# Performance work log

Hardware: AMD Instinct MI355X
Metric: run time of the kernel (lower is better)

The kernel has to match this reference:

```python
import jax, jax.numpy as jnp
import numpy as np

N_NODES = 100000
N_EDGES = 1600000
IN_DIM = 33
HID = 128
N_CLASSES = 10
N_GRAPHS = 128


def _glorot(key, shape):
    fan_in, fan_out = shape[0], shape[1]
    lim = (6.0 / (fan_in + fan_out)) ** 0.5
    return jax.random.uniform(key, shape, jnp.float32, -lim, lim)


def setup_inputs() -> dict:
    key = jax.random.key(0)
    ks = jax.random.split(key, 20)
    x = jax.random.normal(ks[0], (N_NODES, IN_DIM), jnp.float32)
    edge_index = jax.random.randint(ks[1], (2, N_EDGES), 0, N_NODES, jnp.int64)
    edge_w = jax.random.uniform(ks[2], (N_EDGES,), jnp.float32)
    batch = jnp.sort(jax.random.randint(ks[3], (N_NODES,), 0, N_GRAPHS, jnp.int64))
    p = {
        "We": _glorot(ks[4], (IN_DIM, HID)), "be": jnp.zeros((HID,), jnp.float32),
        "W1": _glorot(ks[5], (HID, HID)), "b1": jnp.zeros((HID,), jnp.float32),
        "W2": _glorot(ks[6], (HID, HID)), "b2": jnp.zeros((HID,), jnp.float32),
        "W3": _glorot(ks[7], (HID, HID)), "b3": jnp.zeros((HID,), jnp.float32),
        "W4": _glorot(ks[8], (HID, HID)), "b4": jnp.zeros((HID,), jnp.float32),
        "Wr1": _glorot(ks[9], (HID, HID // 2)), "br1": jnp.zeros((HID // 2,), jnp.float32),
        "Wr2": _glorot(ks[10], (HID // 2, HID // 4)), "br2": jnp.zeros((HID // 4,), jnp.float32),
        "Wr3": _glorot(ks[11], (HID // 4, N_CLASSES)),
    }
    return dict(x=x, edge_index=edge_index, edge_w=edge_w, batch=batch, **p)


def reference(x, edge_index, edge_w, batch,
              We, be, W1, b1, W2, b2, W3, b3, W4, b4,
              Wr1, br1, Wr2, br2, Wr3):
    N = x.shape[0]
    row, col = edge_index[0], edge_index[1]
    # PyG gcn_norm with add_self_loops=True: append (i,i) edges with weight 1
    loop = jnp.arange(N)
    row2 = jnp.concatenate([row, loop])
    col2 = jnp.concatenate([col, loop])
    w2 = jnp.concatenate([edge_w, jnp.ones((N,), edge_w.dtype)])
    deg = jax.ops.segment_sum(w2, col2, num_segments=N)  # in-degree incl. self-loop
    dinv = jnp.where(deg > 0, deg ** -0.5, 0.0)
    norm = dinv[row2] * w2 * dinv[col2]  # [E+N] symmetric normalization

    def conv(h, W, b):
        h = h @ W  # linear transform first (PyG GCNConv)
        msg = norm[:, None] * h[row2]  # gather + scale
        return jax.ops.segment_sum(msg, col2, num_segments=N) + b  # scatter-add to targets

    h = x @ We + be
    h = jax.nn.relu(conv(h, W1, b1))
    h = jax.nn.relu(conv(h, W2, b2))
    h = jax.nn.relu(conv(h, W3, b3))
    h = jax.nn.relu(conv(h, W4, b4))

    # global mean pool over graphs
    sums = jax.ops.segment_sum(h, batch, num_segments=N_GRAPHS)
    cnt = jax.ops.segment_sum(jnp.ones((N,), h.dtype), batch, num_segments=N_GRAPHS)
    pooled = sums / jnp.maximum(cnt, 1.0)[:, None]  # [G, HID]

    r = jax.nn.relu(pooled @ Wr1 + br1)
    r = jax.nn.relu(r @ Wr2 + br2)
    return r @ Wr3  # [G, n_classes]
```

## Files before the change

kernel.cpp:

```cpp
#include <hip/hip_runtime.h>
#include <hip/hip_bf16.h>

#define NN 100000
#define NE 1600000
#define IN_DIM 33
#define HID 128
#define NG 128
#define NCLS 10

using short8 = __attribute__((ext_vector_type(8))) short;
using floatx4 = __attribute__((ext_vector_type(4))) float;

static __device__ __forceinline__ size_t szmul(int a, int b) {
    return (size_t)a * (size_t)b;
}

static __device__ __forceinline__ unsigned short f2bf(float f) {
    unsigned u = __float_as_uint(f);
    u += 0x7fffu + ((u >> 16) & 1u);
    return (unsigned short)(u >> 16);
}
static __device__ __forceinline__ float bf_lo(unsigned u) { return __uint_as_float(u << 16); }
static __device__ __forceinline__ float bf_hi(unsigned u) { return __uint_as_float(u & 0xffff0000u); }

__global__ void k_init(int* bucket_cnt, int* bucket_fill, float* gsum) {
    int i = blockIdx.x * blockDim.x + threadIdx.x;
    if (i < 513) { bucket_cnt[i] = 0; bucket_fill[i] = 0; }
    if (i < NG * HID) gsum[i] = 0.0f;
}


__global__ __launch_bounds__(256) void k_bhist(const int* __restrict__ col,
                                               int* __restrict__ bucket_cnt, int e, int nbk) {
    __shared__ int hist[512];
    int tid = threadIdx.x;
    for (int i = tid; i < nbk; i += 256) hist[i] = 0;
    __syncthreads();
    for (int i = blockIdx.x * 256 + tid; i < e; i += 256 * 256)
        atomicAdd(&hist[col[i] >> 8], 1);
    __syncthreads();
    for (int i = tid; i < nbk; i += 256)
        if (hist[i]) atomicAdd(&bucket_cnt[i], hist[i]);
}

__global__ void k_scan_small(int* data, int nb) {
    __shared__ int s[512];
    int t = threadIdx.x;
    int v = (t < nb) ? data[t] : 0;
    s[t] = v;
    __syncthreads();
    for (int o = 1; o < 512; o <<= 1) {
        int a = (t >= o) ? s[t - o] : 0;
        __syncthreads();
        s[t] += a;
        __syncthreads();
    }
    if (t < nb) data[t] = s[t] - v;
    if (t == nb - 1) data[nb] = s[t];
}

__global__ __launch_bounds__(256) void k_bin_scatter(const int* __restrict__ row,
                                                     const int* __restrict__ col,
                                                     const float* __restrict__ w,
                                                     const int* __restrict__ bucket_base,
                                                     int* __restrict__ bucket_fill,
                                                     uint2* __restrict__ binned, int e, int nbk) {
    __shared__ int hist[512], rnk[512], basub[512];
    int tid = threadIdx.x;
    int c0 = blockIdx.x * 4096;
    for (int i = tid; i < nbk; i += 256) { hist[i] = 0; rnk[i] = 0; }
    __syncthreads();
    int myb[16]; unsigned myp[16]; unsigned myw[16];
#pragma unroll
    for (int u = 0; u < 16; ++u) {
        int idx = c0 + u * 256 + tid;
        int b = -1;
        if (idx < e) {
            int c = col[idx];
            int r = row[idx];
            myw[u] = __float_as_uint(w[idx]);
            b = c >> 8;
            myp[u] = ((unsigned)(c & 255) << 17) | (unsigned)r;
            atomicAdd(&hist[b], 1);
        }
        myb[u] = b;
    }
    __syncthreads();
    for (int i = tid; i < nbk; i += 256) {
        int c = hist[i];
        basub[i] = (c > 0) ? (bucket_base[i] + atomicAdd(&bucket_fill[i], c)) : 0;
    }
    __syncthreads();
#pragma unroll
    for (int u = 0; u < 16; ++u) {
        int b = myb[u];
        if (b >= 0) {
            int rk = atomicAdd(&rnk[b], 1);
            binned[basub[b] + rk] = make_uint2(myp[u], myw[u]);
        }
    }
}

__global__ __launch_bounds__(256) void k_bucket_cnt(const uint2* __restrict__ binned,
                                                    const int* __restrict__ bucket_base,
                                                    int* __restrict__ cnt, int n) {
    __shared__ int c256[256];
    int b = blockIdx.x, tid = threadIdx.x;
    c256[tid] = 0;
    __syncthreads();
    int beg = bucket_base[b], end = bucket_base[b + 1];
    for (int e2 = beg + tid; e2 < end; e2 += 256)
        atomicAdd(&c256[(binned[e2].x >> 17) & 255], 1);
    __syncthreads();
    int node = b * 256 + tid;
    if (node < n) cnt[node] = c256[tid];
}

#define SCAN_B 1024
__global__ void k_scan1(const int* __restrict__ cnt, int* __restrict__ rowptr,
                        int* __restrict__ bsums, int n) {
    __shared__ int s[SCAN_B];
    int t = threadIdx.x;
    int i = blockIdx.x * SCAN_B + t;
    int v = (i < n) ? cnt[i] : 0;
    s[t] = v;
    __syncthreads();
    for (int o = 1; o < SCAN_B; o <<= 1) {
        int a = (t >= o) ? s[t - o] : 0;
        __syncthreads();
        s[t] += a;
        __syncthreads();
    }
    if (i < n) rowptr[i] = s[t] - v;
    if (t == SCAN_B - 1) bsums[blockIdx.x] = s[t];
}

__global__ void k_scan3(int* rowptr, const int* __restrict__ bsums, int n, int etot) {
    int i = blockIdx.x * blockDim.x + threadIdx.x;
    if (i < n) rowptr[i] += bsums[i >> 10];
    else if (i == n) rowptr[n] = etot;
}

__global__ __launch_bounds__(256) void k_bucket_scatter(const uint2* __restrict__ binned,
                                                        const int* __restrict__ bucket_base,
                                                        const int* __restrict__ rowptr,
                                                        int2* __restrict__ csr, int n) {
    __shared__ int f256[256];
    int b = blockIdx.x, tid = threadIdx.x;
    f256[tid] = 0;
    __syncthreads();
    int beg = bucket_base[b], end = bucket_base[b + 1];
    for (int e2 = beg + tid; e2 < end; e2 += 256) {
        uint2 rec = binned[e2];
        int lo = (rec.x >> 17) & 255;
        int node = (b << 8) | lo;
        int src = rec.x & 0x1FFFF;
        int pos = rowptr[node] + atomicAdd(&f256[lo], 1);
        csr[pos] = make_int2(src, (int)rec.y);
    }
    (void)n;
}

__global__ void k_deg(const int* __restrict__ rowptr, const int2* __restrict__ csr,
                      float* __restrict__ dinv, float* __restrict__ selfn, int n) {
    int i = blockIdx.x * blockDim.x + threadIdx.x;
    if (i >= n) return;
    int beg = rowptr[i], end = rowptr[i + 1];
    float d = 1.0f;
    for (int e = beg; e < end; ++e) d += __int_as_float(csr[e].y);
    float di = (d > 0.0f) ? (1.0f / sqrtf(d)) : 0.0f;
    dinv[i] = di;
    selfn[i] = di * di;
}

__global__ void k_norm(const int* __restrict__ rowptr, int2* __restrict__ csr,
                       const float* __restrict__ dinv, int n) {
    int i = blockIdx.x * blockDim.x + threadIdx.x;
    if (i >= n) return;
    float dc = dinv[i];
    int beg = rowptr[i], end = rowptr[i + 1];
    for (int e = beg; e < end; ++e) {
        int2 v = csr[e];
        float nw = dinv[v.x] * __int_as_float(v.y) * dc;
        csr[e] = make_int2(v.x, __float_as_int(nw));
    }
}

__global__ void k_combine(const float* __restrict__ We, const float* __restrict__ W1,
                          const float* __restrict__ be,
                          float* __restrict__ M, float* __restrict__ v) {
    int f = threadIdx.x;
    int k = blockIdx.x;
    if (k < IN_DIM) {
        float a = 0.0f;
#pragma unroll 8
        for (int j = 0; j < HID; ++j) a += We[k * HID + j] * W1[j * HID + f];
        M[k * HID + f] = a;
    } else {
        float a = 0.0f;
#pragma unroll 8
        for (int j = 0; j < HID; ++j) a += be[j] * W1[j * HID + f];
        v[f] = a;
    }
}

__global__ void k_wcast3(const float* __restrict__ W1, const float* __restrict__ W2,
                         const float* __restrict__ W3, unsigned short* __restrict__ Wt) {
    int k = blockIdx.x, c = threadIdx.x, l = blockIdx.y;
    const float* W = (l == 0) ? W1 : (l == 1) ? W2 : W3;
    Wt[((size_t)l * HID + c) * HID + k] = f2bf(W[k * HID + c]);
}

__global__ __launch_bounds__(256) void k_gemm_x(const float* __restrict__ x,
                                                const float* __restrict__ M,
                                                const float* __restrict__ v,
                                                unsigned short* __restrict__ tb, int n) {
    __shared__ float sX[32 * IN_DIM];
    int n0 = blockIdx.x * 32;
    int tid = threadIdx.x;
    int cnt = n - n0; if (cnt > 32) cnt = 32;
    for (int idx = tid; idx < cnt * IN_DIM; idx += 256)
        sX[idx] = x[szmul(n0, IN_DIM) + idx];
    __syncthreads();
    int f = tid & 127, g = tid >> 7;
    float Mc[IN_DIM];
#pragma unroll
    for (int k = 0; k < IN_DIM; ++k) Mc[k] = M[k * HID + f];
    float vf = v[f];
    int ndEnd = g * 16 + 16; if (ndEnd > cnt) ndEnd = cnt;
    for (int nd = g * 16; nd < ndEnd; ++nd) {
        float a = vf;
#pragma unroll
        for (int k = 0; k < IN_DIM; ++k) a += sX[nd * IN_DIM + k] * Mc[k];
        tb[szmul(n0 + nd, HID) + f] = f2bf(a);
    }
}

__global__ __launch_bounds__(256) void k_gemm_mfma(const unsigned short* __restrict__ A,
                                                   const unsigned short* __restrict__ Wt,
                                                   unsigned short* __restrict__ T, int n) {
    int wave = threadIdx.x >> 6;
    int lane = threadIdx.x & 63;
    int r = lane & 15, kg = lane >> 4;
    int row0 = blockIdx.x * 64 + wave * 16;
    int arow = row0 + r;
    short8 af[4];
#pragma unroll
    for (int kk = 0; kk < 4; ++kk) {
        if (arow < n)
            af[kk] = *reinterpret_cast<const short8*>(A + szmul(arow, HID) + kk * 32 + kg * 8);
        else
            af[kk] = short8{0, 0, 0, 0, 0, 0, 0, 0};
    }
#pragma unroll
    for (int ct = 0; ct < 8; ++ct) {
        floatx4 acc = {0.f, 0.f, 0.f, 0.f};
#pragma unroll
        for (int kk = 0; kk < 4; ++kk) {
            short8 bf = *reinterpret_cast<const short8*>(
                Wt + (size_t)(ct * 16 + r) * HID + kk * 32 + kg * 8);
            acc = __builtin_amdgcn_mfma_f32_16x16x32_bf16(af[kk], bf, acc, 0, 0, 0);
        }
#pragma unroll
        for (int reg = 0; reg < 4; ++reg) {
            int orow = row0 + kg * 4 + reg;
            if (orow < n)
                T[szmul(orow, HID) + ct * 16 + r] = f2bf(acc[reg]);
        }
    }
}

__global__ __launch_bounds__(256) void k_aggregate(const uint4* __restrict__ tb,
                                                   const int* __restrict__ rowptr,
                                                   const int2* __restrict__ csr,
                                                   const float* __restrict__ selfn,
                                                   const float* __restrict__ bias,
                                                   uint4* __restrict__ hout, int n) {
    int i = (blockIdx.x * 256 + threadIdx.x) >> 4;
    if (i >= n) return;
    int p = threadIdx.x & 15;
    uint4 sv = tb[szmul(i, 16) + p];
    float sn = selfn[i];
    const float4* bp = reinterpret_cast<const float4*>(bias + p * 8);
    float4 b0 = bp[0], b1 = bp[1];
    float a0 = b0.x + sn * bf_lo(sv.x), a1 = b0.y + sn * bf_hi(sv.x);
    float a2 = b0.z + sn * bf_lo(sv.y), a3 = b0.w + sn * bf_hi(sv.y);
    float a4 = b1.x + sn * bf_lo(sv.z), a5 = b1.y + sn * bf_hi(sv.z);
    float a6 = b1.z + sn * bf_lo(sv.w), a7 = b1.w + sn * bf_hi(sv.w);
    int beg = rowptr[i], end = rowptr[i + 1];
#pragma unroll 4
    for (int j = beg; j < end; ++j) {
        int2 e = csr[j];
        float wj = __int_as_float(e.y);
        uint4 r = tb[szmul(e.x, 16) + p];
        a0 += wj * bf_lo(r.x); a1 += wj * bf_hi(r.x);
        a2 += wj * bf_lo(r.y); a3 += wj * bf_hi(r.y);
        a4 += wj * bf_lo(r.z); a5 += wj * bf_hi(r.z);
        a6 += wj * bf_lo(r.w); a7 += wj * bf_hi(r.w);
    }
    unsigned u0 = (unsigned)f2bf(fmaxf(a0, 0.f)) | ((unsigned)f2bf(fmaxf(a1, 0.f)) << 16);
    unsigned u1 = (unsigned)f2bf(fmaxf(a2, 0.f)) | ((unsigned)f2bf(fmaxf(a3, 0.f)) << 16);
    unsigned u2 = (unsigned)f2bf(fmaxf(a4, 0.f)) | ((unsigned)f2bf(fmaxf(a5, 0.f)) << 16);
    unsigned u3 = (unsigned)f2bf(fmaxf(a6, 0.f)) | ((unsigned)f2bf(fmaxf(a7, 0.f)) << 16);
    hout[szmul(i, 16) + p] = make_uint4(u0, u1, u2, u3);
}

__global__ void k_gcount_bs(const int* __restrict__ batch, int* gcnt, int n) {
    int g = threadIdx.x;
    if (g >= NG) return;
    int lo = 0, hi = n;
    while (lo < hi) { int mid = (lo + hi) >> 1; if (batch[mid] < g) lo = mid + 1; else hi = mid; }
    int start = lo;
    lo = 0; hi = n;
    while (lo < hi) { int mid = (lo + hi) >> 1; if (batch[mid] < g + 1) lo = mid + 1; else hi = mid; }
    gcnt[g] = lo - start;
}

__global__ __launch_bounds__(128) void k_pool(const unsigned short* __restrict__ h,
                                              const int* __restrict__ batch,
                                              float* gsum, int n) {
    int f = threadIdx.x;
    int i0 = blockIdx.x * 32;
    int i1 = min(i0 + 32, n);
    if (i0 >= n) return;
    float acc = 0.0f;
    int cur = batch[i0];
    for (int i = i0; i < i1; ++i) {
        int g = batch[i];
        if (g != cur) { atomicAdd(&gsum[cur * HID + f], acc); acc = 0.0f; cur = g; }
        acc += __uint_as_float((unsigned)h[szmul(i, HID) + f] << 16);
    }
    atomicAdd(&gsum[cur * HID + f], acc);
}

__global__ __launch_bounds__(128) void k_mlp(const float* __restrict__ gsum,
                                             const int* __restrict__ gcnt,
                                             const float* __restrict__ Wr1, const float* __restrict__ br1,
                                             const float* __restrict__ Wr2, const float* __restrict__ br2,
                                             const float* __restrict__ Wr3,
                                             float* __restrict__ out) {
    int g = blockIdx.x;
    int t = threadIdx.x;
    __shared__ float p[HID];
    __shared__ float r1[64];
    __shared__ float r2[32];
    float c = fmaxf((float)gcnt[g], 1.0f);
    p[t] = gsum[g * HID + t] / c;
    __syncthreads();
    if (t < 64) {
        float a = br1[t];
#pragma unroll 8
        for (int k = 0; k < HID; ++k) a += p[k] * Wr1[k * 64 + t];
        r1[t] = fmaxf(a, 0.0f);
    }
    __syncthreads();
    if (t < 32) {
        float a = br2[t];
#pragma unroll 8
        for (int k = 0; k < 64; ++k) a += r1[k] * Wr2[k * 32 + t];
        r2[t] = fmaxf(a, 0.0f);
    }
    __syncthreads();
    if (t < NCLS) {
        float a = 0.0f;
#pragma unroll
        for (int k = 0; k < 32; ++k) a += r2[k] * Wr3[k * NCLS + t];
        out[g * NCLS + t] = a;
    }
}

extern "C" void kernel_launch(void* const* d_in, const int* in_sizes, int n_in,
                              void* d_out, int out_size, void* d_ws, size_t ws_size,
                              hipStream_t stream) {
    const float* x     = (const float*)d_in[0];
    const int*   ei    = (const int*)d_in[1];
    const float* ew    = (const float*)d_in[2];
    const int*   batch = (const int*)d_in[3];
    const float* We  = (const float*)d_in[4];
    const float* be  = (const float*)d_in[5];
    const float* Wl[4] = { (const float*)d_in[6], (const float*)d_in[8],
                           (const float*)d_in[10], (const float*)d_in[12] };
    const float* bl[4] = { (const float*)d_in[7], (const float*)d_in[9],
                           (const float*)d_in[11], (const float*)d_in[13] };
    const float* Wr1 = (const float*)d_in[14];
    const float* br1 = (const float*)d_in[15];
    const float* Wr2 = (const float*)d_in[16];
    const float* br2 = (const float*)d_in[17];
    const float* Wr3 = (const float*)d_in[18];
    float* out = (float*)d_out;

    const int N = in_sizes[3];
    const int E = in_sizes[2];
    const int* row = ei;
    const int* col = ei + E;
    const int nbk = (N + 255) >> 8;

    char* w = (char*)d_ws;
    size_t off = 0;
    auto alloc = [&](size_t bytes) -> void* {
        void* p = w + off;
        off = (off + bytes + 255) & ~(size_t)255;
        return p;
    };
    float* dinv       = (float*)alloc((size_t)N * 4);
    float* selfn      = (float*)alloc((size_t)N * 4);
    int*   cnt        = (int*)  alloc((size_t)N * 4);
    int*   rowptr     = (int*)  alloc((size_t)(N + 1) * 4);
    int*   bsums      = (int*)  alloc(4096);
    int*   bucket_cnt = (int*)  alloc(513 * 4);
    int*   bucket_fill= (int*)  alloc(513 * 4);
    int2*  csr        = (int2*) alloc((size_t)E * 8);
    unsigned short* h  = (unsigned short*)alloc((size_t)N * HID * 2);
    unsigned short* tb = (unsigned short*)alloc((size_t)N * HID * 2);
    unsigned short* Wt = (unsigned short*)alloc((size_t)3 * HID * HID * 2);
    float* M          = (float*)alloc((size_t)IN_DIM * HID * 4);
    float* vbe        = (float*)alloc((size_t)HID * 4);
    float* gsum       = (float*)alloc((size_t)NG * HID * 4);
    int*   gcnt       = (int*)  alloc((size_t)NG * 4);
    uint2* binned     = (uint2*)tb;
    (void)ws_size;

    auto cdiv = [](int a, int b) { return (a + b - 1) / b; };

    k_init<<<64, 256, 0, stream>>>(bucket_cnt, bucket_fill, gsum);
    k_bhist<<<256, 256, 0, stream>>>(col, bucket_cnt, E, nbk);
    k_scan_small<<<1, 512, 0, stream>>>(bucket_cnt, nbk);
    k_bin_scatter<<<cdiv(E, 4096), 256, 0, stream>>>(row, col, ew, bucket_cnt,
                                                     bucket_fill, binned, E, nbk);
    k_bucket_cnt<<<nbk, 256, 0, stream>>>(binned, bucket_cnt, cnt, N);

    int nb = cdiv(N, SCAN_B);
    k_scan1<<<nb, SCAN_B, 0, stream>>>(cnt, rowptr, bsums, N);
    k_scan_small<<<1, 512, 0, stream>>>(bsums, nb);
    k_scan3<<<cdiv(N + 1, 256), 256, 0, stream>>>(rowptr, bsums, N, E);
    k_bucket_scatter<<<nbk, 256, 0, stream>>>(binned, bucket_cnt, rowptr, csr, N);

    k_deg<<<cdiv(N, 256), 256, 0, stream>>>(rowptr, csr, dinv, selfn, N);
    k_norm<<<cdiv(N, 256), 256, 0, stream>>>(rowptr, csr, dinv, N);

    k_combine<<<IN_DIM + 1, HID, 0, stream>>>(We, Wl[0], be, M, vbe);
    k_wcast3<<<dim3(HID, 3), HID, 0, stream>>>(Wl[1], Wl[2], Wl[3], Wt);

    k_gemm_x<<<cdiv(N, 32), 256, 0, stream>>>(x, M, vbe, tb, N);
    k_aggregate<<<cdiv(N, 16), 256, 0, stream>>>((const uint4*)tb, rowptr, csr,
                                                 selfn, bl[0], (uint4*)h, N);

    for (int l = 1; l < 4; ++l) {
        k_gemm_mfma<<<cdiv(N, 64), 256, 0, stream>>>(h, Wt + (size_t)(l - 1) * HID * HID,
                                                     tb, N);
        k_aggregate<<<cdiv(N, 16), 256, 0, stream>>>((const uint4*)tb, rowptr, csr,
                                                     selfn, bl[l], (uint4*)h, N);
    }

    k_gcount_bs<<<1, 128, 0, stream>>>(batch, gcnt, N);
    k_pool<<<cdiv(N, 32), 128, 0, stream>>>(h, batch, gsum, N);
    k_mlp<<<NG, HID, 0, stream>>>(gsum, gcnt, Wr1, br1, Wr2, br2, Wr3, out);

    (void)out_size; (void)n_in;
}
```

Baseline: 514.2 us.

## Fuse degree and normalization into bucket passes; reorder MFMA loops for ILP

The weighted in-degree is now accumulated in shared memory during the bucket count pass, and a small kernel turns it into dinv. The edge normalization is applied while scattering into CSR, so the separate k_deg and k_norm passes over the CSR array go away. The dense MFMA GEMM now keeps 8 accumulators and puts the k loop outside, so independent MFMAs can overlap. This raises register use per thread, and float shared atomics make the degree sums order-dependent.

Result: faster. 500.7 us (-2.6%).

```diff
diff --git a/kernel.cpp b/kernel.cpp
--- a/kernel.cpp
+++ b/kernel.cpp
@@ -103,17 +103,33 @@
 
 __global__ __launch_bounds__(256) void k_bucket_cnt(const uint2* __restrict__ binned,
                                                     const int* __restrict__ bucket_base,
-                                                    int* __restrict__ cnt, int n) {
+                                                    int* __restrict__ cnt,
+                                                    float* __restrict__ wsum, int n) {
     __shared__ int c256[256];
+    __shared__ float s256[256];
     int b = blockIdx.x, tid = threadIdx.x;
     c256[tid] = 0;
+    s256[tid] = 0.0f;
     __syncthreads();
     int beg = bucket_base[b], end = bucket_base[b + 1];
-    for (int e2 = beg + tid; e2 < end; e2 += 256)
-        atomicAdd(&c256[(binned[e2].x >> 17) & 255], 1);
+    for (int e2 = beg + tid; e2 < end; e2 += 256) {
+        uint2 rec = binned[e2];
+        int lo = (rec.x >> 17) & 255;
+        atomicAdd(&c256[lo], 1);
+        atomicAdd(&s256[lo], __uint_as_float(rec.y));
+    }
     __syncthreads();
     int node = b * 256 + tid;
-    if (node < n) cnt[node] = c256[tid];
+    if (node < n) { cnt[node] = c256[tid]; wsum[node] = s256[tid]; }
+}
+
+__global__ void k_dinv(float* __restrict__ dinv, float* __restrict__ selfn, int n) {
+    int i = blockIdx.x * blockDim.x + threadIdx.x;
+    if (i >= n) return;
+    float d = 1.0f + dinv[i];
+    float di = (d > 0.0f) ? (1.0f / sqrtf(d)) : 0.0f;
+    dinv[i] = di;
+    selfn[i] = di * di;
 }
 
 #define SCAN_B 1024
@@ -144,6 +160,7 @@
 __global__ __launch_bounds__(256) void k_bucket_scatter(const uint2* __restrict__ binned,
                                                         const int* __restrict__ bucket_base,
                                                         const int* __restrict__ rowptr,
+                                                        const float* __restrict__ dinv,
                                                         int2* __restrict__ csr, int n) {
     __shared__ int f256[256];
     int b = blockIdx.x, tid = threadIdx.x;
@@ -155,35 +172,11 @@
         int lo = (rec.x >> 17) & 255;
         int node = (b << 8) | lo;
         int src = rec.x & 0x1FFFF;
+        float nw = dinv[src] * __uint_as_float(rec.y) * dinv[node];
         int pos = rowptr[node] + atomicAdd(&f256[lo], 1);
-        csr[pos] = make_int2(src, (int)rec.y);
+        csr[pos] = make_int2(src, __float_as_int(nw));
     }
     (void)n;
-}
-
-__global__ void k_deg(const int* __restrict__ rowptr, const int2* __restrict__ csr,
-                      float* __restrict__ dinv, float* __restrict__ selfn, int n) {
-    int i = blockIdx.x * blockDim.x + threadIdx.x;
-    if (i >= n) return;
-    int beg = rowptr[i], end = rowptr[i + 1];
-    float d = 1.0f;
-    for (int e = beg; e < end; ++e) d += __int_as_float(csr[e].y);
-    float di = (d > 0.0f) ? (1.0f / sqrtf(d)) : 0.0f;
-    dinv[i] = di;
-    selfn[i] = di * di;
-}
-
-__global__ void k_norm(const int* __restrict__ rowptr, int2* __restrict__ csr,
-                       const float* __restrict__ dinv, int n) {
-    int i = blockIdx.x * blockDim.x + threadIdx.x;
-    if (i >= n) return;
-    float dc = dinv[i];
-    int beg = rowptr[i], end = rowptr[i + 1];
-    for (int e = beg; e < end; ++e) {
-        int2 v = csr[e];
-        float nw = dinv[v.x] * __int_as_float(v.y) * dc;
-        csr[e] = make_int2(v.x, __float_as_int(nw));
-    }
 }
 
 __global__ void k_combine(const float* __restrict__ We, const float* __restrict__ W1,
@@ -252,20 +245,25 @@
         else
             af[kk] = short8{0, 0, 0, 0, 0, 0, 0, 0};
     }
-#pragma unroll
-    for (int ct = 0; ct < 8; ++ct) {
-        floatx4 acc = {0.f, 0.f, 0.f, 0.f};
-#pragma unroll
-        for (int kk = 0; kk < 4; ++kk) {
+    floatx4 acc[8];
+#pragma unroll
+    for (int ct = 0; ct < 8; ++ct) acc[ct] = floatx4{0.f, 0.f, 0.f, 0.f};
+#pragma unroll
+    for (int kk = 0; kk < 4; ++kk) {
+#pragma unroll
+        for (int ct = 0; ct < 8; ++ct) {
             short8 bf = *reinterpret_cast<const short8*>(
                 Wt + (size_t)(ct * 16 + r) * HID + kk * 32 + kg * 8);
-            acc = __builtin_amdgcn_mfma_f32_16x16x32_bf16(af[kk], bf, acc, 0, 0, 0);
+            acc[ct] = __builtin_amdgcn_mfma_f32_16x16x32_bf16(af[kk], bf, acc[ct], 0, 0, 0);
         }
+    }
+#pragma unroll
+    for (int ct = 0; ct < 8; ++ct) {
 #pragma unroll
         for (int reg = 0; reg < 4; ++reg) {
             int orow = row0 + kg * 4 + reg;
             if (orow < n)
-                T[szmul(orow, HID) + ct * 16 + r] = f2bf(acc[reg]);
+                T[szmul(orow, HID) + ct * 16 + r] = f2bf(acc[ct][reg]);
         }
     }
 }
@@ -427,16 +425,14 @@
     k_scan_small<<<1, 512, 0, stream>>>(bucket_cnt, nbk);
     k_bin_scatter<<<cdiv(E, 4096), 256, 0, stream>>>(row, col, ew, bucket_cnt,
                                                      bucket_fill, binned, E, nbk);
-    k_bucket_cnt<<<nbk, 256, 0, stream>>>(binned, bucket_cnt, cnt, N);
+    k_bucket_cnt<<<nbk, 256, 0, stream>>>(binned, bucket_cnt, cnt, dinv, N);
+    k_dinv<<<cdiv(N, 256), 256, 0, stream>>>(dinv, selfn, N);
 
     int nb = cdiv(N, SCAN_B);
     k_scan1<<<nb, SCAN_B, 0, stream>>>(cnt, rowptr, bsums, N);
     k_scan_small<<<1, 512, 0, stream>>>(bsums, nb);
     k_scan3<<<cdiv(N + 1, 256), 256, 0, stream>>>(rowptr, bsums, N, E);
-    k_bucket_scatter<<<nbk, 256, 0, stream>>>(binned, bucket_cnt, rowptr, csr, N);
-
-    k_deg<<<cdiv(N, 256), 256, 0, stream>>>(rowptr, csr, dinv, selfn, N);
-    k_norm<<<cdiv(N, 256), 256, 0, stream>>>(rowptr, csr, dinv, N);
+    k_bucket_scatter<<<nbk, 256, 0, stream>>>(binned, bucket_cnt, rowptr, dinv, csr, N);
 
     k_combine<<<IN_DIM + 1, HID, 0, stream>>>(We, Wl[0], be, M, vbe);
     k_wcast3<<<dim3(HID, 3), HID, 0, stream>>>(Wl[1], Wl[2], Wl[3], Wt);
```
